# Kernel optimization log

Hardware: AMD Instinct MI355X
Metric: run time of the kernel (lower is better)

## Reference

```python
import jax, jax.numpy as jnp
import numpy as np

EPS = 1e-6  # flax LayerNorm default

def _layer_norm(x, scale, bias):
    mu = jnp.mean(x, axis=-1, keepdims=True)
    var = jnp.mean(jnp.square(x - mu), axis=-1, keepdims=True)
    return (x - mu) * jax.lax.rsqrt(var + EPS) * scale + bias

def setup_inputs() -> dict:
    key = jax.random.key(0)
    ks = jax.random.split(key, 8)
    B, S, D_in, D_h, D_out, N = 4, 2048, 1024, 2048, 1024, 6
    init = lambda k, shape, fan_in: jax.random.normal(k, shape, jnp.float32) / np.sqrt(fan_in)
    return {
        "x": jax.random.normal(ks[0], (B, S, D_in), jnp.float32),
        "ln1_scale": jnp.ones((D_in,), jnp.float32),
        "ln1_bias": jnp.zeros((D_in,), jnp.float32),
        "w1": init(ks[1], (D_in, D_h), D_in),
        "b1": jnp.zeros((D_h,), jnp.float32),
        "block_ln_scales": jnp.ones((N, D_h), jnp.float32),
        "block_ln_biases": jnp.zeros((N, D_h), jnp.float32),
        "block_ws": init(ks[2], (N, D_h, D_h), D_h),
        "block_bs": jnp.zeros((N, D_h), jnp.float32),
        "ln2_scale": jnp.ones((D_h,), jnp.float32),
        "ln2_bias": jnp.zeros((D_h,), jnp.float32),
        "w2": init(ks[3], (D_h, D_out), D_h),
        "b2": jnp.zeros((D_out,), jnp.float32),
    }

def reference(x, ln1_scale, ln1_bias, w1, b1, block_ln_scales, block_ln_biases,
              block_ws, block_bs, ln2_scale, ln2_bias, w2, b2):
    # stem: LN -> Linear -> SiLU
    h = _layer_norm(x, ln1_scale, ln1_bias)
    h = jax.nn.silu(jnp.einsum('bsd,dh->bsh', h, w1) + b1)

    # residual blocks via scan over stacked params
    def block(h, params):
        s, b, w, lb = params
        y = _layer_norm(h, s, b)
        y = jax.nn.silu(jnp.einsum('bsh,hk->bsk', y, w) + lb)
        return h + y, None

    h, _ = jax.lax.scan(block, h, (block_ln_scales, block_ln_biases, block_ws, block_bs))

    # head: LN -> Linear
    h = _layer_norm(h, ln2_scale, ln2_bias)
    return jnp.einsum('bsh,ho->bso', h, w2) + b2
```

## Files before the change

### kernel.cpp

```cpp
#include <hip/hip_runtime.h>
#include <hip/hip_bf16.h>

typedef short short8 __attribute__((ext_vector_type(8)));
typedef float f32x4 __attribute__((ext_vector_type(4)));

#define AS1(p) ((const __attribute__((address_space(1))) void*)(p))
#define AS3(p) ((__attribute__((address_space(3))) void*)(p))

__device__ __forceinline__ ushort f2bf(float f) {
  __hip_bfloat16 h = __float2bfloat16(f);
  return *reinterpret_cast<const ushort*>(&h);
}

__device__ __forceinline__ float silu_f(float v) { return v / (1.f + __expf(-v)); }

template<int NV>
__global__ __launch_bounds__(256) void ln_bf16_k(
    const float* __restrict__ in, const float* __restrict__ sc,
    const float* __restrict__ bi, ushort* __restrict__ out)
{
  const int D = NV * 1024;
  const long row = blockIdx.x;
  const int tx = threadIdx.x;
  const float* p = in + row * (long)D;
  float4 v[NV];
  float s = 0.f, s2 = 0.f;
#pragma unroll
  for (int t = 0; t < NV; ++t) {
    v[t] = *reinterpret_cast<const float4*>(p + t * 1024 + tx * 4);
    s  += v[t].x + v[t].y + v[t].z + v[t].w;
    s2 += v[t].x * v[t].x + v[t].y * v[t].y + v[t].z * v[t].z + v[t].w * v[t].w;
  }
#pragma unroll
  for (int o = 1; o < 64; o <<= 1) { s += __shfl_xor(s, o); s2 += __shfl_xor(s2, o); }
  __shared__ float red[2][4];
  const int wave = tx >> 6;
  if ((tx & 63) == 0) { red[0][wave] = s; red[1][wave] = s2; }
  __syncthreads();
  s  = red[0][0] + red[0][1] + red[0][2] + red[0][3];
  s2 = red[1][0] + red[1][1] + red[1][2] + red[1][3];
  const float mu   = s / D;
  const float rstd = rsqrtf(s2 / D - mu * mu + 1e-6f);
#pragma unroll
  for (int t = 0; t < NV; ++t) {
    const int d = t * 1024 + tx * 4;
    float4 g = *reinterpret_cast<const float4*>(sc + d);
    float4 b = *reinterpret_cast<const float4*>(bi + d);
    ushort4 o;
    o.x = f2bf((v[t].x - mu) * rstd * g.x + b.x);
    o.y = f2bf((v[t].y - mu) * rstd * g.y + b.y);
    o.z = f2bf((v[t].z - mu) * rstd * g.z + b.z);
    o.w = f2bf((v[t].w - mu) * rstd * g.w + b.w);
    *reinterpret_cast<ushort4*>(out + row * (long)D + d) = o;
  }
}

__global__ __launch_bounds__(256) void transpose_bf16_k(
    const float* __restrict__ in, ushort* __restrict__ out, int K, int N)
{
  __shared__ float tile[64][65];
  const int k0 = blockIdx.y * 64, n0 = blockIdx.x * 64;
  const int tx = threadIdx.x, ty = threadIdx.y;
#pragma unroll
  for (int r = ty; r < 64; r += 4)
    tile[r][tx] = in[(long)(k0 + r) * N + n0 + tx];
  __syncthreads();
#pragma unroll
  for (int r = ty; r < 64; r += 4)
    out[(long)(n0 + r) * K + k0 + tx] = f2bf(tile[tx][r]);
}

#define STG(gsrc, ldst)                                                          \
  __builtin_amdgcn_global_load_lds(AS1(gsrc),          AS3(ldst),        16, 0, 0); \
  __builtin_amdgcn_global_load_lds(AS1((gsrc) + offQ), AS3((ldst) + 8192), 16, 0, 0);

#define ldsA(B, H) (ldsW + (B) * 65536 + (H) * 16384)
#define ldsB(B, H) (ldsW + (B) * 65536 + 32768 + (H) * 16384)

#define LOAD_A(dst, DB, ihalf)                                                  \
  _Pragma("unroll") for (int i_ = 0; i_ < 4; ++i_) {                            \
    dst[i_][0] = *(const short8*)(smem + (DB) * 65536 + aOff + ((ihalf) * 4 + i_) * 2048 + rdk0); \
    dst[i_][1] = *(const short8*)(smem + (DB) * 65536 + aOff + ((ihalf) * 4 + i_) * 2048 + rdk1); \
  }

#define LOAD_B(dst, DB, jhalf)                                                  \
  _Pragma("unroll") for (int j_ = 0; j_ < 2; ++j_) {                            \
    dst[j_][0] = *(const short8*)(smem + (DB) * 65536 + bOff + ((jhalf) * 2 + j_) * 2048 + rdk0); \
    dst[j_][1] = *(const short8*)(smem + (DB) * 65536 + bOff + ((jhalf) * 2 + j_) * 2048 + rdk1); \
  }

#define MFMA_Q(ihalf, jhalf, afr, bfr)                                          \
  __builtin_amdgcn_s_setprio(1);                                                \
  _Pragma("unroll") for (int kk_ = 0; kk_ < 2; ++kk_)                           \
  _Pragma("unroll") for (int i_ = 0; i_ < 4; ++i_)                              \
  _Pragma("unroll") for (int j_ = 0; j_ < 2; ++j_)                              \
    acc[(ihalf) * 4 + i_][(jhalf) * 2 + j_] =                                   \
        __builtin_amdgcn_mfma_f32_16x16x32_bf16(afr[i_][kk_], bfr[j_][kk_],     \
            acc[(ihalf) * 4 + i_][(jhalf) * 2 + j_], 0, 0, 0);                  \
  __builtin_amdgcn_s_setprio(0);

#define DO_TILE(CUR, NXT, AO1, AO2, BO2, S0, S2, S3, TAILW)                     \
  LOAD_A(af, CUR, 0);                                                           \
  LOAD_B(bf0, CUR, 0);                                                          \
  if (S0) { STG(aP + (AO1) + offH, ldsA(NXT, 1)); }                             \
  __builtin_amdgcn_s_barrier();                                                 \
  MFMA_Q(0, 0, af, bf0);                                                        \
  __builtin_amdgcn_s_barrier();                                                 \
  LOAD_B(bf1, CUR, 1);                                                          \
  __builtin_amdgcn_s_barrier();                                                 \
  MFMA_Q(0, 1, af, bf1);                                                        \
  __builtin_amdgcn_s_barrier();                                                 \
  LOAD_A(af, CUR, 1);                                                           \
  if (S2) { STG(bP + (BO2), ldsB(CUR, 0)); }                                    \
  __builtin_amdgcn_s_barrier();                                                 \
  MFMA_Q(1, 1, af, bf1);                                                        \
  __builtin_amdgcn_s_barrier();                                                 \
  if (S3) { STG(bP + (BO2) + offH, ldsB(CUR, 1)); STG(aP + (AO2), ldsA(CUR, 0)); } \
  if (S3)            { asm volatile("s_waitcnt vmcnt(6)" ::: "memory"); }       \
  else if (TAILW)    { asm volatile("s_waitcnt vmcnt(0)" ::: "memory"); }       \
  __builtin_amdgcn_sched_barrier(0);                                            \
  __builtin_amdgcn_s_barrier();                                                 \
  MFMA_Q(1, 0, af, bf0);                                                        \
  __builtin_amdgcn_s_barrier();

template<int MODE>
__global__ __launch_bounds__(512, 2) void gemm256_k(
    const ushort* __restrict__ A, const ushort* __restrict__ Bt,
    const float* __restrict__ bias, float* __restrict__ C,
    int M, int N, int K)
{
  extern __shared__ char smem[];
  const int tid = threadIdx.x;
  const int lane = tid & 63, wid = tid >> 6;
  const int wr = wid >> 2, wc = wid & 3;
  const int nbx = N >> 8;

  int bid;
  {
    const int b = blockIdx.x;
    const int cpx = gridDim.x >> 3;
    bid = (b & 7) * cpx + (b >> 3);
  }
  const int bx = bid % nbx, by = bid / nbx;
  const long m0 = (long)by << 8, n0 = (long)bx << 8;

  const int srow = tid >> 3;
  const int scol = (((tid & 7) * 16) ^ (((tid >> 3) & 7) << 4)) >> 1;
  const ushort* aP = A  + (m0 + srow) * (long)K + scol;
  const ushort* bP = Bt + (n0 + srow) * (long)K + scol;
  const long offH = 128L * K, offQ = 64L * K;
  char* ldsW = smem + wid * 1024;

  const int rdk0 = (((lane >> 4) * 16)     ) ^ ((lane & 7) << 4);
  const int rdk1 = (((lane >> 4) * 16) + 64) ^ ((lane & 7) << 4);
  const int aOff = wr * 16384 + (lane & 15) * 128;
  const int bOff = 32768 + (wc >> 1) * 16384 + ((wc & 1) * 64 + (lane & 15)) * 128;

  f32x4 acc[8][4] = {};
  const int NT = K >> 6;

  STG(aP,           ldsA(0, 0));  STG(aP + offH,      ldsA(0, 1));
  STG(bP,           ldsB(0, 0));  STG(bP + offH,      ldsB(0, 1));
  STG(bP + 64,      ldsB(1, 0));  STG(bP + 64 + offH, ldsB(1, 1));
  STG(aP + 64,      ldsA(1, 0));
  asm volatile("s_waitcnt vmcnt(6)" ::: "memory");
  __builtin_amdgcn_sched_barrier(0);
  __builtin_amdgcn_s_barrier();

  short8 af[4][2], bf0[2][2], bf1[2][2];
  for (int t = 0; t < NT - 2; t += 2) {
    DO_TILE(0, 1,  64, 128, 128, 1, 1, 1, 0)
    DO_TILE(1, 0, 128, 192, 192, 1, 1, 1, 0)
    aP += 128; bP += 128;
  }
  DO_TILE(0, 1, 64, 0, 0, 1, 0, 0, 1)
  DO_TILE(1, 0,  0, 0, 0, 0, 0, 0, 0)

#pragma unroll
  for (int j = 0; j < 4; ++j) {
    const long col = n0 + wc * 64 + j * 16 + (lane & 15);
    const float bj = bias[col];
#pragma unroll
    for (int i = 0; i < 8; ++i) {
      const long rowb = m0 + wr * 128 + i * 16 + ((lane >> 4) << 2);
#pragma unroll
      for (int r = 0; r < 4; ++r) {
        float v = acc[i][j][r] + bj;
        const long idx = (rowb + r) * N + col;
        if (MODE == 0)      C[idx] = silu_f(v);
        else if (MODE == 1) C[idx] = C[idx] + silu_f(v);
        else                C[idx] = v;
      }
    }
  }
}

extern "C" void kernel_launch(void* const* d_in, const int* in_sizes, int n_in,
                              void* d_out, int out_size, void* d_ws, size_t ws_size,
                              hipStream_t stream) {
  const float* x     = (const float*)d_in[0];
  const float* ln1_s = (const float*)d_in[1];
  const float* ln1_b = (const float*)d_in[2];
  const float* w1    = (const float*)d_in[3];
  const float* b1    = (const float*)d_in[4];
  const float* bln_s = (const float*)d_in[5];
  const float* bln_b = (const float*)d_in[6];
  const float* bws   = (const float*)d_in[7];
  const float* bbs   = (const float*)d_in[8];
  const float* ln2_s = (const float*)d_in[9];
  const float* ln2_b = (const float*)d_in[10];
  const float* w2    = (const float*)d_in[11];
  const float* b2    = (const float*)d_in[12];
  float* out = (float*)d_out;

  const int M = 8192;
  char* ws = (char*)d_ws;
  float*  h   = (float*)ws;
  ushort* Abf = (ushort*)(ws + 67108864);
  ushort* wt  = (ushort*)(ws + 67108864 + 33554432);
  const long W1T = 0;
  const long BLK = 2097152;
  const long W2T = BLK + 6L * 4194304;

  (void)hipFuncSetAttribute((const void*)gemm256_k<0>,
      hipFuncAttributeMaxDynamicSharedMemorySize, 131072);
  (void)hipFuncSetAttribute((const void*)gemm256_k<1>,
      hipFuncAttributeMaxDynamicSharedMemorySize, 131072);
  (void)hipFuncSetAttribute((const void*)gemm256_k<2>,
      hipFuncAttributeMaxDynamicSharedMemorySize, 131072);

  dim3 tb(64, 4);
  transpose_bf16_k<<<dim3(2048 / 64, 1024 / 64), tb, 0, stream>>>(w1, wt + W1T, 1024, 2048);
  for (int i = 0; i < 6; ++i)
    transpose_bf16_k<<<dim3(32, 32), tb, 0, stream>>>(
        bws + (long)i * 2048 * 2048, wt + BLK + (long)i * 4194304, 2048, 2048);
  transpose_bf16_k<<<dim3(1024 / 64, 2048 / 64), tb, 0, stream>>>(w2, wt + W2T, 2048, 1024);

  ln_bf16_k<1><<<M, 256, 0, stream>>>(x, ln1_s, ln1_b, Abf);
  gemm256_k<0><<<32 * 8, 512, 131072, stream>>>(Abf, wt + W1T, b1, h, M, 2048, 1024);

  for (int i = 0; i < 6; ++i) {
    ln_bf16_k<2><<<M, 256, 0, stream>>>(h, bln_s + i * 2048, bln_b + i * 2048, Abf);
    gemm256_k<1><<<32 * 8, 512, 131072, stream>>>(
        Abf, wt + BLK + (long)i * 4194304, bbs + i * 2048, h, M, 2048, 2048);
  }

  ln_bf16_k<2><<<M, 256, 0, stream>>>(h, ln2_s, ln2_b, Abf);
  gemm256_k<2><<<32 * 4, 512, 131072, stream>>>(Abf, wt + W2T, b2, out, M, 1024, 2048);
}
```

Before: 798.3 us.

## Store residual stream in bf16 and prefetch next B fragments across tiles

The residual hidden state h moves from fp32 to bf16. This halves the bytes read and written by the layernorm kernels and by the residual read-modify-write in the GEMM epilogue, and a new bf16-input layernorm kernel is added for it. The GEMM main loop also reorders its LDS reads so that B fragments for the next tile are loaded after the last MFMA quarter, which removes two barriers per tile. The cost is precision: residual accumulation across six blocks now rounds to bf16 each time, and the prefetch adds register pressure.

```diff
diff --git a/kernel.cpp b/kernel.cpp
--- a/kernel.cpp
+++ b/kernel.cpp
@@ -11,7 +11,12 @@
   __hip_bfloat16 h = __float2bfloat16(f);
   return *reinterpret_cast<const ushort*>(&h);
 }
-
+__device__ __forceinline__ float bfu2f(ushort u) {
+  unsigned int x = ((unsigned int)u) << 16;
+  float f;
+  __builtin_memcpy(&f, &x, 4);
+  return f;
+}
 __device__ __forceinline__ float silu_f(float v) { return v / (1.f + __expf(-v)); }
 
 template<int NV>
@@ -55,6 +60,44 @@
   }
 }
 
+__global__ __launch_bounds__(256) void ln_bf16b_k(
+    const ushort* __restrict__ in, const float* __restrict__ sc,
+    const float* __restrict__ bi, ushort* __restrict__ out)
+{
+  const long row = blockIdx.x;
+  const int tx = threadIdx.x;
+  const int d = tx * 8;
+  short8 v8 = *reinterpret_cast<const short8*>(in + row * 2048 + d);
+  float v[8];
+  float s = 0.f, s2 = 0.f;
+#pragma unroll
+  for (int j = 0; j < 8; ++j) {
+    v[j] = bfu2f((ushort)v8[j]);
+    s += v[j]; s2 += v[j] * v[j];
+  }
+#pragma unroll
+  for (int o = 1; o < 64; o <<= 1) { s += __shfl_xor(s, o); s2 += __shfl_xor(s2, o); }
+  __shared__ float red[2][4];
+  const int wave = tx >> 6;
+  if ((tx & 63) == 0) { red[0][wave] = s; red[1][wave] = s2; }
+  __syncthreads();
+  s  = red[0][0] + red[0][1] + red[0][2] + red[0][3];
+  s2 = red[1][0] + red[1][1] + red[1][2] + red[1][3];
+  const float mu   = s * (1.f / 2048.f);
+  const float rstd = rsqrtf(s2 * (1.f / 2048.f) - mu * mu + 1e-6f);
+  float4 g0 = *reinterpret_cast<const float4*>(sc + d);
+  float4 g1 = *reinterpret_cast<const float4*>(sc + d + 4);
+  float4 b0 = *reinterpret_cast<const float4*>(bi + d);
+  float4 b1 = *reinterpret_cast<const float4*>(bi + d + 4);
+  const float gg[8] = {g0.x, g0.y, g0.z, g0.w, g1.x, g1.y, g1.z, g1.w};
+  const float bb[8] = {b0.x, b0.y, b0.z, b0.w, b1.x, b1.y, b1.z, b1.w};
+  short8 o8;
+#pragma unroll
+  for (int j = 0; j < 8; ++j)
+    o8[j] = (short)f2bf((v[j] - mu) * rstd * gg[j] + bb[j]);
+  *reinterpret_cast<short8*>(out + row * 2048 + d) = o8;
+}
+
 __global__ __launch_bounds__(256) void transpose_bf16_k(
     const float* __restrict__ in, ushort* __restrict__ out, int K, int N)
 {
@@ -99,34 +142,31 @@
             acc[(ihalf) * 4 + i_][(jhalf) * 2 + j_], 0, 0, 0);                  \
   __builtin_amdgcn_s_setprio(0);
 
-#define DO_TILE(CUR, NXT, AO1, AO2, BO2, S0, S2, S3, TAILW)                     \
+#define DO_TILE(CUR, NXT, BA, BB, AO1, AO2, BO2, S0, S2, S3, TAILW, PFB)        \
   LOAD_A(af, CUR, 0);                                                           \
-  LOAD_B(bf0, CUR, 0);                                                          \
   if (S0) { STG(aP + (AO1) + offH, ldsA(NXT, 1)); }                             \
   __builtin_amdgcn_s_barrier();                                                 \
-  MFMA_Q(0, 0, af, bf0);                                                        \
-  __builtin_amdgcn_s_barrier();                                                 \
-  LOAD_B(bf1, CUR, 1);                                                          \
-  __builtin_amdgcn_s_barrier();                                                 \
-  MFMA_Q(0, 1, af, bf1);                                                        \
+  MFMA_Q(0, 0, af, BA);                                                         \
+  MFMA_Q(0, 1, af, BB);                                                         \
   __builtin_amdgcn_s_barrier();                                                 \
   LOAD_A(af, CUR, 1);                                                           \
   if (S2) { STG(bP + (BO2), ldsB(CUR, 0)); }                                    \
   __builtin_amdgcn_s_barrier();                                                 \
-  MFMA_Q(1, 1, af, bf1);                                                        \
+  MFMA_Q(1, 1, af, BB);                                                         \
   __builtin_amdgcn_s_barrier();                                                 \
   if (S3) { STG(bP + (BO2) + offH, ldsB(CUR, 1)); STG(aP + (AO2), ldsA(CUR, 0)); } \
   if (S3)            { asm volatile("s_waitcnt vmcnt(6)" ::: "memory"); }       \
   else if (TAILW)    { asm volatile("s_waitcnt vmcnt(0)" ::: "memory"); }       \
   __builtin_amdgcn_sched_barrier(0);                                            \
   __builtin_amdgcn_s_barrier();                                                 \
-  MFMA_Q(1, 0, af, bf0);                                                        \
+  MFMA_Q(1, 0, af, BA);                                                         \
+  if (PFB) { LOAD_B(BB, NXT, 0); LOAD_B(BA, NXT, 1); }                          \
   __builtin_amdgcn_s_barrier();
 
 template<int MODE>
 __global__ __launch_bounds__(512, 2) void gemm256_k(
     const ushort* __restrict__ A, const ushort* __restrict__ Bt,
-    const float* __restrict__ bias, float* __restrict__ C,
+    const float* __restrict__ bias, void* __restrict__ Cv,
     int M, int N, int K)
 {
   extern __shared__ char smem[];
@@ -167,14 +207,17 @@
   __builtin_amdgcn_sched_barrier(0);
   __builtin_amdgcn_s_barrier();
 
-  short8 af[4][2], bf0[2][2], bf1[2][2];
+  short8 af[4][2], bfA[2][2], bfB[2][2];
+  LOAD_B(bfA, 0, 0);
+  LOAD_B(bfB, 0, 1);
+
   for (int t = 0; t < NT - 2; t += 2) {
-    DO_TILE(0, 1,  64, 128, 128, 1, 1, 1, 0)
-    DO_TILE(1, 0, 128, 192, 192, 1, 1, 1, 0)
+    DO_TILE(0, 1, bfA, bfB,  64, 128, 128, 1, 1, 1, 0, 1)
+    DO_TILE(1, 0, bfB, bfA, 128, 192, 192, 1, 1, 1, 0, 1)
     aP += 128; bP += 128;
   }
-  DO_TILE(0, 1, 64, 0, 0, 1, 0, 0, 1)
-  DO_TILE(1, 0,  0, 0, 0, 0, 0, 0, 0)
+  DO_TILE(0, 1, bfA, bfB, 64, 0, 0, 1, 0, 0, 1, 1)
+  DO_TILE(1, 0, bfB, bfA,  0, 0, 0, 0, 0, 0, 0, 0)
 
 #pragma unroll
   for (int j = 0; j < 4; ++j) {
@@ -185,11 +228,16 @@
       const long rowb = m0 + wr * 128 + i * 16 + ((lane >> 4) << 2);
 #pragma unroll
       for (int r = 0; r < 4; ++r) {
-        float v = acc[i][j][r] + bj;
+        const float v = acc[i][j][r] + bj;
         const long idx = (rowb + r) * N + col;
-        if (MODE == 0)      C[idx] = silu_f(v);
-        else if (MODE == 1) C[idx] = C[idx] + silu_f(v);
-        else                C[idx] = v;
+        if (MODE == 0) {
+          ((ushort*)Cv)[idx] = f2bf(silu_f(v));
+        } else if (MODE == 1) {
+          ushort* C = (ushort*)Cv;
+          C[idx] = f2bf(bfu2f(C[idx]) + silu_f(v));
+        } else {
+          ((float*)Cv)[idx] = v;
+        }
       }
     }
   }
@@ -215,9 +263,9 @@
 
   const int M = 8192;
   char* ws = (char*)d_ws;
-  float*  h   = (float*)ws;
-  ushort* Abf = (ushort*)(ws + 67108864);
-  ushort* wt  = (ushort*)(ws + 67108864 + 33554432);
+  ushort* h   = (ushort*)ws;
+  ushort* Abf = (ushort*)(ws + 33554432);
+  ushort* wt  = (ushort*)(ws + 67108864);
   const long W1T = 0;
   const long BLK = 2097152;
   const long W2T = BLK + 6L * 4194304;
@@ -237,14 +285,14 @@
   transpose_bf16_k<<<dim3(1024 / 64, 2048 / 64), tb, 0, stream>>>(w2, wt + W2T, 2048, 1024);
 
   ln_bf16_k<1><<<M, 256, 0, stream>>>(x, ln1_s, ln1_b, Abf);
-  gemm256_k<0><<<32 * 8, 512, 131072, stream>>>(Abf, wt + W1T, b1, h, M, 2048, 1024);
+  gemm256_k<0><<<32 * 8, 512, 131072, stream>>>(Abf, wt + W1T, b1, (void*)h, M, 2048, 1024);
 
   for (int i = 0; i < 6; ++i) {
-    ln_bf16_k<2><<<M, 256, 0, stream>>>(h, bln_s + i * 2048, bln_b + i * 2048, Abf);
+    ln_bf16b_k<<<M, 256, 0, stream>>>(h, bln_s + i * 2048, bln_b + i * 2048, Abf);
     gemm256_k<1><<<32 * 8, 512, 131072, stream>>>(
-        Abf, wt + BLK + (long)i * 4194304, bbs + i * 2048, h, M, 2048, 2048);
-  }
-
-  ln_bf16_k<2><<<M, 256, 0, stream>>>(h, ln2_s, ln2_b, Abf);
-  gemm256_k<2><<<32 * 4, 512, 131072, stream>>>(Abf, wt + W2T, b2, out, M, 1024, 2048);
-}
+        Abf, wt + BLK + (long)i * 4194304, bbs + i * 2048, (void*)h, M, 2048, 2048);
+  }
+
+  ln_bf16b_k<<<M, 256, 0, stream>>>(h, ln2_s, ln2_b, Abf);
+  gemm256_k<2><<<32 * 4, 512, 131072, stream>>>(Abf, wt + W2T, b2, (void*)out, M, 1024, 2048);
+}
```

Measured after the change: 755.8 us. -5.3%, faster.
